# Kernel optimization log

Hardware: AMD Instinct MI355X
Metric: run time of the kernel (lower is better)

## Reference

```python
import jax, jax.numpy as jnp
import numpy as np

B, H, I, O, T = 256, 1024, 1, 512, 512


def setup_inputs() -> dict:
    key = jax.random.key(0)
    ks = jax.random.split(key, 7)
    sc = 1.0 / np.sqrt(H).astype(np.float32)
    rn = lambda k, shape, s=1.0: (jax.random.normal(k, shape, jnp.float32) * s)
    return {
        "z": rn(ks[0], (B, H)),
        "w_ih": rn(ks[1], (4 * H, I), sc),
        "w_hh": rn(ks[2], (4 * H, H), sc),
        "b_ih": rn(ks[3], (4 * H,), sc),
        "b_hh": rn(ks[4], (4 * H,), sc),
        "w_lin": rn(ks[5], (O, H), sc),
        "b_lin": rn(ks[6], (O,), sc),
        "seq_length": T,
    }


def reference(z, w_ih, w_hh, b_ih, b_hh, w_lin, b_lin, seq_length):
    # next input is argmax of the linear head (greedy feedback, in_features==1).
    batch = z.shape[0]
    in_feat = w_ih.shape[1]
    bias = b_ih + b_hh

    def step(carry, _):
        h, c, xin = carry
        gates = xin @ w_ih.T + h @ w_hh.T + bias  # [B, 4H], torch gate order i,f,g,o
        i, f, g, o = jnp.split(gates, 4, axis=-1)
        c = jax.nn.sigmoid(f) * c + jax.nn.sigmoid(i) * jnp.tanh(g)
        h = jax.nn.sigmoid(o) * jnp.tanh(c)
        x_t = h @ w_lin.T + b_lin  # [B, O]
        nxt = jnp.argmax(x_t, axis=-1).astype(z.dtype).reshape(batch, in_feat)
        return (h, c, nxt), x_t

    init = (z, jnp.zeros_like(z), jnp.zeros((batch, in_feat), z.dtype))
    _, ys = jax.lax.scan(step, init, None, length=seq_length)  # [T, B, O]
    return jnp.transpose(ys, (1, 0, 2))  # [B, T, O]
```

## Files before the change

kernel.cpp:

```cpp
#include <hip/hip_runtime.h>
#include <math.h>
#include <float.h>

#define NB 256
#define NH 1024
#define NO 512
#define NT 512

#define OFF_HT4_0 0
#define OFF_HT4_1 (256*1024)
#define OFF_CT    (2*256*1024)
#define OFF_WLT   (3*256*1024)
#define OFF_PART  (OFF_WLT + 512*1024)
#define OFF_BAR   (OFF_PART + 8192)

__device__ __forceinline__ float sigf(float x) { return 1.f / (1.f + expf(-x)); }

#define FMA4(A, W, H4) \
  A = fmaf((W).x, (H4).x, A); A = fmaf((W).y, (H4).y, A); \
  A = fmaf((W).z, (H4).z, A); A = fmaf((W).w, (H4).w, A);

__global__ void k_init(const float* __restrict__ z, const float* __restrict__ w_lin,
                       float* __restrict__ ws) {
  int idx = blockIdx.x * 256 + threadIdx.x;
  if (idx < 512 * 1024) {
    int j = idx & 3, o = (idx >> 2) & 511, uq = idx >> 11;
    ws[OFF_WLT + idx] = w_lin[o * 1024 + (uq << 2) + j];
  }
  if (idx < 256 * 1024) {
    int q = idx >> 10, r = idx & 1023, b = r >> 2, j = r & 3;
    ws[OFF_HT4_0 + idx] = z[b * 1024 + (q << 2) + j];
    ws[OFF_CT + idx] = 0.f;
  }
  if (idx < 8192) ws[OFF_PART + idx] = (idx & 1) ? 0.f : -FLT_MAX;
  if (idx < 256) ((unsigned*)(ws + OFF_BAR))[idx] = 0u;
}

__device__ __forceinline__ void gbar(unsigned* bar, int bid) {
  __syncthreads();
  if (threadIdx.x == 0) {
    unsigned* gen = bar + 160;
    unsigned g = __hip_atomic_load(gen, __ATOMIC_RELAXED, __HIP_MEMORY_SCOPE_AGENT);
    unsigned* c = bar + ((bid & 7) << 4);
    unsigned a = __hip_atomic_fetch_add(c, 1u, __ATOMIC_ACQ_REL, __HIP_MEMORY_SCOPE_AGENT);
    bool done = false;
    if (a == 31u) {
      __hip_atomic_store(c, 0u, __ATOMIC_RELAXED, __HIP_MEMORY_SCOPE_AGENT);
      unsigned m = __hip_atomic_fetch_add(bar + 128, 1u, __ATOMIC_ACQ_REL,
                                          __HIP_MEMORY_SCOPE_AGENT);
      if (m == 7u) {
        __hip_atomic_store(bar + 128, 0u, __ATOMIC_RELAXED, __HIP_MEMORY_SCOPE_AGENT);
        __hip_atomic_fetch_add(gen, 1u, __ATOMIC_RELEASE, __HIP_MEMORY_SCOPE_AGENT);
        done = true;
      }
    }
    if (!done) {
      while (__hip_atomic_load(gen, __ATOMIC_RELAXED, __HIP_MEMORY_SCOPE_AGENT) == g)
        __builtin_amdgcn_s_sleep(2);
    }
    __builtin_amdgcn_fence(__ATOMIC_ACQUIRE, "agent");
  }
  __syncthreads();
}

__global__ __launch_bounds__(1024, 4) void k_persist(
    const float* __restrict__ w_hh, const float* __restrict__ w_ih,
    const float* __restrict__ b_ih, const float* __restrict__ b_hh,
    const float* __restrict__ b_lin, float* __restrict__ out,
    float* __restrict__ ws) {
  __shared__ float wlds[16 * 1024];
  __shared__ float sh[16 * 1028];
  __shared__ float xpart[8 * 512];

  const int tid = threadIdx.x;
  const int blk = blockIdx.x;
  const int lane = tid & 63;
  const int wid = tid >> 6;

  const int rg = wid & 3;
  const int kh = wid >> 2;

  const int oc = blk & 15, bc = blk >> 4;
  const int kh8 = wid & 7, bh = wid >> 3;
  const int ol = lane & 31, bs = lane >> 5;

  unsigned* bar = (unsigned*)(ws + OFF_BAR);
  float* part = ws + OFF_PART;
  float* cT = ws + OFF_CT;
  const float* wlt = ws + OFF_WLT;

#pragma unroll
  for (int i = 0; i < 4; ++i) {
    int idx = (i << 10) + tid;
    int r = idx >> 8, c4 = idx & 255;
    int grow = ((r & 3) << 10) + (blk << 2) + (r >> 2);
    *(float4*)(&wlds[(r << 10) + (c4 << 2)]) =
        *(const float4*)(w_hh + (grow << 10) + (c4 << 2));
  }

  const int uue = tid & 3;
  const int be = tid >> 2;
  const int ue = (blk << 2) + uue;
  const float bi_ = b_ih[ue] + b_hh[ue];
  const float bf_ = b_ih[1024 + ue] + b_hh[1024 + ue];
  const float bg_ = b_ih[2048 + ue] + b_hh[2048 + ue];
  const float bo_ = b_ih[3072 + ue] + b_hh[3072 + ue];
  const float wi_ = w_ih[ue], wf_ = w_ih[1024 + ue];
  const float wg_ = w_ih[2048 + ue], wo_ = w_ih[3072 + ue];

  const int oo = (oc << 5) + (tid & 31);
  const int ob = (bc << 4) + (tid >> 5);
  const float blr = b_lin[(oc << 5) + (tid & 31)];
  float* outp = out + (long)ob * (NT * NO) + oo;
  const float* wpH = wlt + ((kh8 << 5) << 11) + (((oc << 5) + ol) << 2);
  const float* hpH = &sh[((bh << 3) + (bs << 2)) * 1028 + (kh8 << 7)];

  __syncthreads();

  auto head_phase = [&](const float* __restrict__ hprev, int tout) {
#pragma unroll
    for (int i = 0; i < 4; ++i) {
      int idx = (i << 10) + tid;
      int q = idx >> 4, bb = idx & 15;
      *(float4*)(&sh[bb * 1028 + (q << 2)]) =
          *(const float4*)(hprev + (q << 10) + (((bc << 4) + bb) << 2));
    }
    __syncthreads();
    float pa[4] = {0.f, 0.f, 0.f, 0.f};
#pragma unroll 4
    for (int ug = 0; ug < 32; ++ug) {
      const float4 wv = *(const float4*)(wpH + (ug << 11));
#pragma unroll
      for (int pp = 0; pp < 4; ++pp) {
        const float4 hv = *(const float4*)(hpH + pp * 1028 + (ug << 2));
        FMA4(pa[pp], wv, hv);
      }
    }
#pragma unroll
    for (int pp = 0; pp < 4; ++pp)
      xpart[(kh8 << 9) + (((bh << 3) + (bs << 2) + pp) << 5) + ol] = pa[pp];
    __syncthreads();
    if (tid < 512) {
      float a = blr;
#pragma unroll
      for (int kk = 0; kk < 8; ++kk) a += xpart[(kk << 9) + tid];
      outp[tout << 9] = a;
      float v = a, io = (float)oo;
#pragma unroll
      for (int m = 16; m >= 1; m >>= 1) {
        const float vo = __shfl_xor(v, m, 64);
        const float ioo = __shfl_xor(io, m, 64);
        if (vo > v || (vo == v && ioo < io)) { v = vo; io = ioo; }
      }
      if ((tid & 31) == 0)
        *(float2*)(part + (ob << 5) + (oc << 1)) = make_float2(v, io);
    }
  };

  for (int t = 0; t <= NT; ++t) {
    const float* hcur = ws + ((t & 1) ? OFF_HT4_1 : OFF_HT4_0);
    float* hnext = ws + ((t & 1) ? OFF_HT4_0 : OFF_HT4_1);

    if (t > 0) head_phase(hcur, t - 1);
    if (t == NT) break;

    float acc[4][4];
#pragma unroll
    for (int j = 0; j < 4; ++j)
#pragma unroll
      for (int bb = 0; bb < 4; ++bb) acc[j][bb] = 0.f;
    {
      const float* hq = hcur + (kh << 16) + (lane << 2);
      const float* wb = &wlds[((rg << 2) << 10) + (kh << 8)];
      float4 hA[4], hB[4];
#pragma unroll
      for (int bb = 0; bb < 4; ++bb) hA[bb] = *(const float4*)(hq + (bb << 8));
      for (int qg = 0; qg < 64; qg += 2) {
        if ((qg & 7) == 0) __builtin_amdgcn_s_barrier();
#pragma unroll
        for (int bb = 0; bb < 4; ++bb)
          hB[bb] = *(const float4*)(hq + ((qg + 1) << 10) + (bb << 8));
#pragma unroll
        for (int j = 0; j < 4; ++j) {
          const float4 wv = *(const float4*)(wb + (j << 10) + (qg << 2));
#pragma unroll
          for (int bb = 0; bb < 4; ++bb) { FMA4(acc[j][bb], wv, hA[bb]); }
        }
        if (qg + 2 < 64) {
#pragma unroll
          for (int bb = 0; bb < 4; ++bb)
            hA[bb] = *(const float4*)(hq + ((qg + 2) << 10) + (bb << 8));
        }
#pragma unroll
        for (int j = 0; j < 4; ++j) {
          const float4 wv = *(const float4*)(wb + (j << 10) + ((qg + 1) << 2));
#pragma unroll
          for (int bb = 0; bb < 4; ++bb) { FMA4(acc[j][bb], wv, hB[bb]); }
        }
      }
    }
#pragma unroll
    for (int j = 0; j < 4; ++j)
#pragma unroll
      for (int bb = 0; bb < 4; ++bb)
        sh[(kh << 12) + (((rg << 2) + j) << 8) + (bb << 6) + lane] = acc[j][bb];

    gbar(bar, blk);

    {
      const float* pb = part + (be << 5);
      float4 p0 = *(const float4*)(pb);
      float v = p0.x, ix = p0.y;
      if (p0.z > v) { v = p0.z; ix = p0.w; }
#pragma unroll
      for (int cc = 1; cc < 8; ++cc) {
        float4 p2 = *(const float4*)(pb + (cc << 2));
        if (p2.x > v) { v = p2.x; ix = p2.y; }
        if (p2.z > v) { v = p2.z; ix = p2.w; }
      }
      const float xb = ix;
      const int rb = uue << 10;
      float s0 = 0.f, s1 = 0.f, s2 = 0.f, s3 = 0.f;
#pragma unroll
      for (int kk = 0; kk < 4; ++kk) {
        const int base = (kk << 12) + rb + be;
        s0 += sh[base];
        s1 += sh[base + 256];
        s2 += sh[base + 512];
        s3 += sh[base + 768];
      }
      const float gi = s0 + bi_ + xb * wi_;
      const float gf = s1 + bf_ + xb * wf_;
      const float gg = s2 + bg_ + xb * wg_;
      const float go = s3 + bo_ + xb * wo_;
      const float co = cT[(ue << 8) + be];
      const float cn = sigf(gf) * co + sigf(gi) * tanhf(gg);
      const float hn = sigf(go) * tanhf(cn);
      cT[(ue << 8) + be] = cn;
      hnext[(blk << 10) + tid] = hn;
    }
    gbar(bar, blk);
  }
}

extern "C" void kernel_launch(void* const* d_in, const int* in_sizes, int n_in,
                              void* d_out, int out_size, void* d_ws, size_t ws_size,
                              hipStream_t stream) {
  (void)in_sizes; (void)n_in; (void)out_size; (void)ws_size;
  const float* z     = (const float*)d_in[0];
  const float* w_ih  = (const float*)d_in[1];
  const float* w_hh  = (const float*)d_in[2];
  const float* b_ih  = (const float*)d_in[3];
  const float* b_hh  = (const float*)d_in[4];
  const float* w_lin = (const float*)d_in[5];
  const float* b_lin = (const float*)d_in[6];
  float* out = (float*)d_out;
  float* ws  = (float*)d_ws;

  k_init<<<2048, 256, 0, stream>>>(z, w_lin, ws);

  void* args[] = {(void*)&w_hh, (void*)&w_ih, (void*)&b_ih, (void*)&b_hh,
                  (void*)&b_lin, (void*)&out, (void*)&ws};
  hipLaunchCooperativeKernel((const void*)k_persist, dim3(256), dim3(1024),
                             args, 0, stream);
}
```

Baseline: 33.30 ms.

## Restructure LSTM step: register cell state, wider row tiles, fused head from global h

Keeps the LSTM cell state in a register per thread instead of round-tripping it through the global workspace each step. The recurrent matmul now gives each warp 8 gate rows over a 128-wide K slice instead of 4 rows over 256, and reduces the K-split partials in LDS with two passes. The output-head phase now runs after the gate matmul and reads h directly from global memory instead of staging it into LDS first, which removes one copy and one barrier. The trade-off is more accumulator registers and an extra syncthreads for the partial reduction.

```diff
diff --git a/kernel.cpp b/kernel.cpp
--- a/kernel.cpp
+++ b/kernel.cpp
@@ -9,8 +9,7 @@
 
 #define OFF_HT4_0 0
 #define OFF_HT4_1 (256*1024)
-#define OFF_CT    (2*256*1024)
-#define OFF_WLT   (3*256*1024)
+#define OFF_WLT   (2*256*1024)
 #define OFF_PART  (OFF_WLT + 512*1024)
 #define OFF_BAR   (OFF_PART + 8192)
 
@@ -30,7 +29,6 @@
   if (idx < 256 * 1024) {
     int q = idx >> 10, r = idx & 1023, b = r >> 2, j = r & 3;
     ws[OFF_HT4_0 + idx] = z[b * 1024 + (q << 2) + j];
-    ws[OFF_CT + idx] = 0.f;
   }
   if (idx < 8192) ws[OFF_PART + idx] = (idx & 1) ? 0.f : -FLT_MAX;
   if (idx < 256) ((unsigned*)(ws + OFF_BAR))[idx] = 0u;
@@ -69,24 +67,23 @@
     const float* __restrict__ b_lin, float* __restrict__ out,
     float* __restrict__ ws) {
   __shared__ float wlds[16 * 1024];
-  __shared__ float sh[16 * 1028];
-  __shared__ float xpart[8 * 512];
+  __shared__ float ex[4 * 4096];
+  __shared__ float hx[8 * 512];
 
   const int tid = threadIdx.x;
   const int blk = blockIdx.x;
   const int lane = tid & 63;
   const int wid = tid >> 6;
 
-  const int rg = wid & 3;
-  const int kh = wid >> 2;
+  const int rg = wid >> 3;
+  const int kq = wid & 7;
 
   const int oc = blk & 15, bc = blk >> 4;
-  const int kh8 = wid & 7, bh = wid >> 3;
-  const int ol = lane & 31, bs = lane >> 5;
+  const int kh = wid & 7, bh = wid >> 3;
+  const int bsel = lane >> 5, ol = lane & 31;
 
   unsigned* bar = (unsigned*)(ws + OFF_BAR);
   float* part = ws + OFF_PART;
-  float* cT = ws + OFF_CT;
   const float* wlt = ws + OFF_WLT;
 
 #pragma unroll
@@ -95,115 +92,131 @@
     int r = idx >> 8, c4 = idx & 255;
     int grow = ((r & 3) << 10) + (blk << 2) + (r >> 2);
     *(float4*)(&wlds[(r << 10) + (c4 << 2)]) =
-        *(const float4*)(w_hh + (grow << 10) + (c4 << 2));
-  }
-
-  const int uue = tid & 3;
+        *(const float4*)(w_hh + ((long)grow << 10) + (c4 << 2));
+  }
+
+  const int uu = tid & 3;
   const int be = tid >> 2;
-  const int ue = (blk << 2) + uue;
+  const int ue = (blk << 2) + uu;
   const float bi_ = b_ih[ue] + b_hh[ue];
   const float bf_ = b_ih[1024 + ue] + b_hh[1024 + ue];
   const float bg_ = b_ih[2048 + ue] + b_hh[2048 + ue];
   const float bo_ = b_ih[3072 + ue] + b_hh[3072 + ue];
   const float wi_ = w_ih[ue], wf_ = w_ih[1024 + ue];
   const float wg_ = w_ih[2048 + ue], wo_ = w_ih[3072 + ue];
+  float creg = 0.f;
 
   const int oo = (oc << 5) + (tid & 31);
   const int ob = (bc << 4) + (tid >> 5);
   const float blr = b_lin[(oc << 5) + (tid & 31)];
   float* outp = out + (long)ob * (NT * NO) + oo;
-  const float* wpH = wlt + ((kh8 << 5) << 11) + (((oc << 5) + ol) << 2);
-  const float* hpH = &sh[((bh << 3) + (bs << 2)) * 1028 + (kh8 << 7)];
+
+  const float* wrow = &wlds[rg << 13];
 
   __syncthreads();
 
-  auto head_phase = [&](const float* __restrict__ hprev, int tout) {
-#pragma unroll
-    for (int i = 0; i < 4; ++i) {
-      int idx = (i << 10) + tid;
-      int q = idx >> 4, bb = idx & 15;
-      *(float4*)(&sh[bb * 1028 + (q << 2)]) =
-          *(const float4*)(hprev + (q << 10) + (((bc << 4) + bb) << 2));
-    }
-    __syncthreads();
-    float pa[4] = {0.f, 0.f, 0.f, 0.f};
-#pragma unroll 4
-    for (int ug = 0; ug < 32; ++ug) {
-      const float4 wv = *(const float4*)(wpH + (ug << 11));
-#pragma unroll
-      for (int pp = 0; pp < 4; ++pp) {
-        const float4 hv = *(const float4*)(hpH + pp * 1028 + (ug << 2));
-        FMA4(pa[pp], wv, hv);
-      }
-    }
-#pragma unroll
-    for (int pp = 0; pp < 4; ++pp)
-      xpart[(kh8 << 9) + (((bh << 3) + (bs << 2) + pp) << 5) + ol] = pa[pp];
-    __syncthreads();
-    if (tid < 512) {
-      float a = blr;
-#pragma unroll
-      for (int kk = 0; kk < 8; ++kk) a += xpart[(kk << 9) + tid];
-      outp[tout << 9] = a;
-      float v = a, io = (float)oo;
-#pragma unroll
-      for (int m = 16; m >= 1; m >>= 1) {
-        const float vo = __shfl_xor(v, m, 64);
-        const float ioo = __shfl_xor(io, m, 64);
-        if (vo > v || (vo == v && ioo < io)) { v = vo; io = ioo; }
-      }
-      if ((tid & 31) == 0)
-        *(float2*)(part + (ob << 5) + (oc << 1)) = make_float2(v, io);
-    }
-  };
-
   for (int t = 0; t <= NT; ++t) {
-    const float* hcur = ws + ((t & 1) ? OFF_HT4_1 : OFF_HT4_0);
-    float* hnext = ws + ((t & 1) ? OFF_HT4_0 : OFF_HT4_1);
-
-    if (t > 0) head_phase(hcur, t - 1);
+    const float* hin = ws + ((t & 1) ? OFF_HT4_1 : OFF_HT4_0);
+    float* hout = ws + ((t & 1) ? OFF_HT4_0 : OFF_HT4_1);
+
+    if (t < NT) {
+      float acc[8][4];
+#pragma unroll
+      for (int j = 0; j < 8; ++j)
+#pragma unroll
+        for (int bb = 0; bb < 4; ++bb) acc[j][bb] = 0.f;
+
+      const float* hq = hin + ((kq << 5) << 10) + (lane << 2);
+      float4 hA[4], hB[4];
+#pragma unroll
+      for (int bb = 0; bb < 4; ++bb) hA[bb] = *(const float4*)(hq + (bb << 8));
+
+      for (int qi = 0; qi < 32; qi += 2) {
+        if ((qi & 7) == 0) __builtin_amdgcn_s_barrier();
+#pragma unroll
+        for (int bb = 0; bb < 4; ++bb)
+          hB[bb] = *(const float4*)(hq + ((qi + 1) << 10) + (bb << 8));
+        {
+          const int ko = ((kq << 5) + qi) << 2;
+#pragma unroll
+          for (int j = 0; j < 8; ++j) {
+            const float4 wv = *(const float4*)(wrow + (j << 10) + ko);
+            FMA4(acc[j][0], wv, hA[0]); FMA4(acc[j][1], wv, hA[1]);
+            FMA4(acc[j][2], wv, hA[2]); FMA4(acc[j][3], wv, hA[3]);
+          }
+        }
+        if (qi + 2 < 32) {
+#pragma unroll
+          for (int bb = 0; bb < 4; ++bb)
+            hA[bb] = *(const float4*)(hq + ((qi + 2) << 10) + (bb << 8));
+        }
+        {
+          const int ko = ((kq << 5) + qi + 1) << 2;
+#pragma unroll
+          for (int j = 0; j < 8; ++j) {
+            const float4 wv = *(const float4*)(wrow + (j << 10) + ko);
+            FMA4(acc[j][0], wv, hB[0]); FMA4(acc[j][1], wv, hB[1]);
+            FMA4(acc[j][2], wv, hB[2]); FMA4(acc[j][3], wv, hB[3]);
+          }
+        }
+      }
+
+      if (kq < 4) {
+#pragma unroll
+        for (int j = 0; j < 8; ++j)
+#pragma unroll
+          for (int bb = 0; bb < 4; ++bb)
+            ex[(kq << 12) + (((rg << 3) + j) << 8) + (bb << 6) + lane] = acc[j][bb];
+      }
+      __syncthreads();
+      if (kq >= 4) {
+        const int p = kq & 3;
+#pragma unroll
+        for (int j = 0; j < 8; ++j)
+#pragma unroll
+          for (int bb = 0; bb < 4; ++bb) {
+            const int a = (p << 12) + (((rg << 3) + j) << 8) + (bb << 6) + lane;
+            ex[a] += acc[j][bb];
+          }
+      }
+      __syncthreads();
+    }
+
+    if (t > 0) {
+      float ah[4] = {0.f, 0.f, 0.f, 0.f};
+      const float* hh = hin + ((kh << 5) << 10);
+      const float* wl = wlt + ((kh << 5) << 11) + (((oc << 5) + ol) << 2);
+#pragma unroll 2
+      for (int qi = 0; qi < 32; ++qi) {
+        const float4 wv = *(const float4*)(wl + (qi << 11));
+#pragma unroll
+        for (int bb = 0; bb < 4; ++bb) {
+          const float4 hv = *(const float4*)(
+              hh + (qi << 10) + (((bc << 4) + (bh << 3) + (bsel << 2) + bb) << 2));
+          FMA4(ah[bb], wv, hv);
+        }
+      }
+#pragma unroll
+      for (int bb = 0; bb < 4; ++bb)
+        hx[(kh << 9) + (((bh << 3) + (bsel << 2) + bb) << 5) + ol] = ah[bb];
+      __syncthreads();
+      if (tid < 512) {
+        float a = blr;
+#pragma unroll
+        for (int kk = 0; kk < 8; ++kk) a += hx[(kk << 9) + tid];
+        outp[(long)(t - 1) << 9] = a;
+        float v = a, io = (float)oo;
+#pragma unroll
+        for (int m = 16; m >= 1; m >>= 1) {
+          const float vo = __shfl_xor(v, m, 64);
+          const float ioo = __shfl_xor(io, m, 64);
+          if (vo > v || (vo == v && ioo < io)) { v = vo; io = ioo; }
+        }
+        if ((tid & 31) == 0)
+          *(float2*)(part + (ob << 5) + (oc << 1)) = make_float2(v, io);
+      }
+    }
     if (t == NT) break;
-
-    float acc[4][4];
-#pragma unroll
-    for (int j = 0; j < 4; ++j)
-#pragma unroll
-      for (int bb = 0; bb < 4; ++bb) acc[j][bb] = 0.f;
-    {
-      const float* hq = hcur + (kh << 16) + (lane << 2);
-      const float* wb = &wlds[((rg << 2) << 10) + (kh << 8)];
-      float4 hA[4], hB[4];
-#pragma unroll
-      for (int bb = 0; bb < 4; ++bb) hA[bb] = *(const float4*)(hq + (bb << 8));
-      for (int qg = 0; qg < 64; qg += 2) {
-        if ((qg & 7) == 0) __builtin_amdgcn_s_barrier();
-#pragma unroll
-        for (int bb = 0; bb < 4; ++bb)
-          hB[bb] = *(const float4*)(hq + ((qg + 1) << 10) + (bb << 8));
-#pragma unroll
-        for (int j = 0; j < 4; ++j) {
-          const float4 wv = *(const float4*)(wb + (j << 10) + (qg << 2));
-#pragma unroll
-          for (int bb = 0; bb < 4; ++bb) { FMA4(acc[j][bb], wv, hA[bb]); }
-        }
-        if (qg + 2 < 64) {
-#pragma unroll
-          for (int bb = 0; bb < 4; ++bb)
-            hA[bb] = *(const float4*)(hq + ((qg + 2) << 10) + (bb << 8));
-        }
-#pragma unroll
-        for (int j = 0; j < 4; ++j) {
-          const float4 wv = *(const float4*)(wb + (j << 10) + ((qg + 1) << 2));
-#pragma unroll
-          for (int bb = 0; bb < 4; ++bb) { FMA4(acc[j][bb], wv, hB[bb]); }
-        }
-      }
-    }
-#pragma unroll
-    for (int j = 0; j < 4; ++j)
-#pragma unroll
-      for (int bb = 0; bb < 4; ++bb)
-        sh[(kh << 12) + (((rg << 2) + j) << 8) + (bb << 6) + lane] = acc[j][bb];
 
     gbar(bar, blk);
 
@@ -219,25 +232,20 @@
         if (p2.z > v) { v = p2.z; ix = p2.w; }
       }
       const float xb = ix;
-      const int rb = uue << 10;
-      float s0 = 0.f, s1 = 0.f, s2 = 0.f, s3 = 0.f;
-#pragma unroll
-      for (int kk = 0; kk < 4; ++kk) {
-        const int base = (kk << 12) + rb + be;
-        s0 += sh[base];
-        s1 += sh[base + 256];
-        s2 += sh[base + 512];
-        s3 += sh[base + 768];
-      }
-      const float gi = s0 + bi_ + xb * wi_;
-      const float gf = s1 + bf_ + xb * wf_;
-      const float gg = s2 + bg_ + xb * wg_;
-      const float go = s3 + bo_ + xb * wo_;
-      const float co = cT[(ue << 8) + be];
-      const float cn = sigf(gf) * co + sigf(gi) * tanhf(gg);
+      float s[4];
+#pragma unroll
+      for (int g = 0; g < 4; ++g) {
+        const int rowoff = (((uu << 2) + g) << 8) + be;
+        s[g] = ex[rowoff] + ex[4096 + rowoff] + ex[8192 + rowoff] + ex[12288 + rowoff];
+      }
+      const float gi = s[0] + bi_ + xb * wi_;
+      const float gf = s[1] + bf_ + xb * wf_;
+      const float gg = s[2] + bg_ + xb * wg_;
+      const float go = s[3] + bo_ + xb * wo_;
+      const float cn = sigf(gf) * creg + sigf(gi) * tanhf(gg);
       const float hn = sigf(go) * tanhf(cn);
-      cT[(ue << 8) + be] = cn;
-      hnext[(blk << 10) + tid] = hn;
+      creg = cn;
+      hout[(blk << 10) + tid] = hn;
     }
     gbar(bar, blk);
   }
```

After: 42.32 ms. +27.1%, slower.
